# Optimization experiments

Measured on AMD Instinct MI355X. Metric: run time of the kernel, lower is better.

The kernel has to match this reference:

```python
import jax, jax.numpy as jnp
import numpy as np

K = 10  # num_neighbors in original nn_index call


def setup_inputs() -> dict:
    key = jax.random.key(0)
    k1, k2, k3, k4 = jax.random.split(key, 4)
    B, OBS, ACT, N = 256, 32, 2, 500000
    obs = jax.random.normal(k1, (B, OBS), dtype=jnp.float32)
    action = jax.random.normal(k2, (B, ACT), dtype=jnp.float32)
    mem_sa = jax.random.normal(k3, (N, OBS + ACT), dtype=jnp.float32)
    mem_Q = jax.random.normal(k4, (N, 1), dtype=jnp.float32)
    return {"obs": obs, "action": action, "mem_sa": mem_sa, "mem_Q": mem_Q}


def reference(obs, action, mem_sa, mem_Q):
    # query: [B, D] state-action, brute-force kNN over memory table [N, D]
    q = jnp.concatenate([obs, action], axis=1)
    # squared Euclidean distances (FLANN returns squared L2): [B, N]
    d2 = (jnp.sum(q * q, axis=1, keepdims=True)
          - 2.0 * q @ mem_sa.T
          + jnp.sum(mem_sa * mem_sa, axis=1)[None, :])
    neg_d, idx = jax.lax.top_k(-d2, K)   # nearest K neighbors
    dists = -neg_d                        # [B, K], ascending
    Qs = mem_Q[idx, 0]                    # gather Q values: [B, K]
    # NOTE: original applies softmax to raw distances (not negated)
    weights = jax.nn.softmax(dists, axis=1)
    return jnp.sum(weights * Qs, axis=1)  # [B]
```

## Files before the change

kernel.cpp:

```cpp
#include <hip/hip_runtime.h>
#include <hip/hip_bf16.h>
#include <math.h>

#define NPTS   500000
#define NB     256
#define TOPK   10
#define CAP    2048
#define SBLK   1024
#define SPER   16
#define MARGIN 2.0f
#define NWCH   15625
#define FBLK   1024
#define NSEG   4
#define LCAP   8
#define PMAIN  393216
#define OCAP   32768
#define CHB    4352

typedef short v2s  __attribute__((ext_vector_type(2)));
typedef short v4s  __attribute__((ext_vector_type(4)));
typedef short v8s  __attribute__((ext_vector_type(8)));
typedef float v16f __attribute__((ext_vector_type(16)));

__device__ __forceinline__ unsigned short f2bf(float f) {
    unsigned u = __float_as_uint(f);
    unsigned r = u + 0x7FFFu + ((u >> 16) & 1u);
    return (unsigned short)(r >> 16);
}
__device__ __forceinline__ float bf2f(unsigned short h) {
    return __uint_as_float(((unsigned)h) << 16);
}
__device__ __forceinline__ v2s pk2(float2 f) {
    __hip_bfloat162 h = __float22bfloat162_rn(f);
    v2s r;
    __builtin_memcpy(&r, &h, 4);
    return r;
}

__device__ __forceinline__ float norm34(const float* __restrict__ r) {
    float a0 = 0.f, a1 = 0.f, a2 = 0.f, a3 = 0.f;
#pragma unroll
    for (int d = 0; d < 32; d += 4) {
        a0 = fmaf(r[d + 0], r[d + 0], a0);
        a1 = fmaf(r[d + 1], r[d + 1], a1);
        a2 = fmaf(r[d + 2], r[d + 2], a2);
        a3 = fmaf(r[d + 3], r[d + 3], a3);
    }
    a0 = fmaf(r[32], r[32], a0);
    a1 = fmaf(r[33], r[33], a1);
    return (a0 + a1) + (a2 + a3);
}
__device__ __forceinline__ float dot34(const float* __restrict__ r, const float* q) {
    float a0 = 0.f, a1 = 0.f, a2 = 0.f, a3 = 0.f;
#pragma unroll
    for (int d = 0; d < 32; d += 4) {
        a0 = fmaf(r[d + 0], q[d + 0], a0);
        a1 = fmaf(r[d + 1], q[d + 1], a1);
        a2 = fmaf(r[d + 2], q[d + 2], a2);
        a3 = fmaf(r[d + 3], q[d + 3], a3);
    }
    a0 = fmaf(r[32], q[32], a0);
    a1 = fmaf(r[33], q[33], a1);
    return (a0 + a1) + (a2 + a3);
}
__device__ __forceinline__ float dot34_v4(const float4* __restrict__ r4, const float* q) {
    float a0 = 0.f, a1 = 0.f, a2 = 0.f, a3 = 0.f;
#pragma unroll
    for (int dp = 0; dp < 8; ++dp) {
        float4 v = r4[dp];
        a0 = fmaf(v.x, q[4 * dp + 0], a0);
        a1 = fmaf(v.y, q[4 * dp + 1], a1);
        a2 = fmaf(v.z, q[4 * dp + 2], a2);
        a3 = fmaf(v.w, q[4 * dp + 3], a3);
    }
    float2 t = *(const float2*)(r4 + 8);
    a0 = fmaf(t.x, q[32], a0);
    a1 = fmaf(t.y, q[33], a1);
    return (a0 + a1) + (a2 + a3);
}
__device__ __forceinline__ void load_q(const float* __restrict__ obs,
                                       const float* __restrict__ act, int b, float* q) {
#pragma unroll
    for (int d = 0; d < 32; ++d) q[d] = obs[b * 32 + d];
    q[32] = act[b * 2 + 0];
    q[33] = act[b * 2 + 1];
}

__global__ __launch_bounds__(256, 4) void k_sample(const float* __restrict__ obs,
                                                   const float* __restrict__ act,
                                                   const float* __restrict__ msa,
                                                   float* __restrict__ minima) {
    __shared__ __align__(16) float sm[SPER * 36];
    __shared__ float smn[SPER];
    const int g = blockIdx.x, t = threadIdx.x;
    const int base = g * SPER;
    for (int i = t; i < SPER * 34; i += 256) {
        int row = i / 34, d = i - row * 34;
        sm[row * 36 + d] = msa[(size_t)base * 34 + i];
    }
    __syncthreads();
    if (t < SPER) smn[t] = norm34(&sm[t * 36]);
    __syncthreads();
    float q[34];
    load_q(obs, act, t, q);
    float best = __builtin_inff();
#pragma unroll
    for (int j = 0; j < SPER; ++j) {
        float s = fmaf(-2.f, dot34_v4((const float4*)&sm[j * 36], q), smn[j]);
        best = fminf(best, s);
    }
    minima[(size_t)t * SBLK + g] = best;
}

__global__ __launch_bounds__(64) void k_tau(const float* __restrict__ minima,
                                            const float* __restrict__ obs,
                                            const float* __restrict__ act,
                                            v8s* __restrict__ afrag,
                                            int* __restrict__ cursor) {
    __shared__ __align__(16) unsigned short qs[48];
    const int b = blockIdx.x, lane = threadIdx.x;
    if (b == 0 && lane == 0) { cursor[0] = 0; cursor[1] = 0; }
    float v[16];
#pragma unroll
    for (int k = 0; k < 16; ++k) v[k] = minima[(size_t)b * SBLK + lane + 64 * k];
    float last = 0.f;
    for (int r = 0; r < TOPK; ++r) {
        float lm = v[0]; int la = 0;
#pragma unroll
        for (int k = 1; k < 16; ++k) { if (v[k] < lm) { lm = v[k]; la = k; } }
        float wm = lm;
        for (int off = 32; off; off >>= 1) wm = fminf(wm, __shfl_xor(wm, off));
        unsigned long long msk = __ballot(lm == wm);
        int first = (int)__builtin_ctzll(msk);
        if (lane == first) {
#pragma unroll
            for (int k = 0; k < 16; ++k) { if (k == la) v[k] = __builtin_inff(); }
        }
        last = wm;
    }
    float val = 0.f;
    if (lane < 32)       val = obs[b * 32 + lane];
    else if (lane < 34)  val = act[b * 2 + (lane - 32)];
    else if (lane == 34) val = -0.5f;
    else if (lane == 35) val = 0.5f * (last + MARGIN);
    if (lane < 48) qs[lane] = (lane < 36) ? f2bf(val) : (unsigned short)0;
    __syncthreads();
    if (lane < 6) {
        int s = lane >> 1, half = lane & 1;
        int qt = b >> 5, mrow = b & 31;
        v8s frag = *(const v8s*)&qs[s * 16 + half * 8];
        afrag[(qt * 3 + s) * 64 + half * 32 + mrow] = frag;
    }
}

__global__ __launch_bounds__(256, 4) void k_filter(const float* __restrict__ msa,
                                                   const v8s* __restrict__ afrag,
                                                   int* __restrict__ cursor,
                                                   unsigned* __restrict__ pbuf,
                                                   int* __restrict__ posq) {
    __shared__ __align__(16) float chunk[2][CHB / 4];
    __shared__ int lcount[NB];
    __shared__ int lcand[NB * LCAP];
    __shared__ int gbase;
    const int g = blockIdx.x, t = threadIdx.x;
    const int w = t >> 6, lane = t & 63;
    const int mrow = lane & 31, half = lane >> 5;
    v8s A[2][3];
#pragma unroll
    for (int j = 0; j < 2; ++j)
#pragma unroll
        for (int s = 0; s < 3; ++s)
            A[j][s] = afrag[((w * 2 + j) * 3 + s) * 64 + lane];
    lcount[t] = 0;
    const v16f zacc = (v16f)0.0f;

    float4 sreg; float treg = 0.f;
    const char* mb = (const char*)msa;
    auto stage_load = [&](int c) {
        const char* cb = mb + (size_t)c * CHB;
        sreg = *(const float4*)(cb + t * 16);
        if (t < 64) treg = *(const float*)(cb + 4096 + t * 4);
    };
    auto stage_write = [&](int nb) {
        *(float4*)((char*)&chunk[nb][0] + t * 16) = sreg;
        if (t < 64) *(float*)((char*)&chunk[nb][0] + 4096 + t * 4) = treg;
    };
    auto process = [&](int cur, int c) {
        const float* rp = &chunk[cur][0] + mrow * 34;
        const int p0 = c * 32 + mrow;
        float2 e0 = *(const float2*)(rp + half * 8 + 0);
        float2 e1 = *(const float2*)(rp + half * 8 + 2);
        float2 e2 = *(const float2*)(rp + half * 8 + 4);
        float2 e3 = *(const float2*)(rp + half * 8 + 6);
        float2 e4 = *(const float2*)(rp + 16 + half * 8 + 0);
        float2 e5 = *(const float2*)(rp + 16 + half * 8 + 2);
        float2 e6 = *(const float2*)(rp + 16 + half * 8 + 4);
        float2 e7 = *(const float2*)(rp + 16 + half * 8 + 6);
        float2 e8 = *(const float2*)(rp + 32);
        float n0 = 0.f, n1 = 0.f;
        n0 = fmaf(e0.x, e0.x, n0); n1 = fmaf(e0.y, e0.y, n1);
        n0 = fmaf(e1.x, e1.x, n0); n1 = fmaf(e1.y, e1.y, n1);
        n0 = fmaf(e2.x, e2.x, n0); n1 = fmaf(e2.y, e2.y, n1);
        n0 = fmaf(e3.x, e3.x, n0); n1 = fmaf(e3.y, e3.y, n1);
        n0 = fmaf(e4.x, e4.x, n0); n1 = fmaf(e4.y, e4.y, n1);
        n0 = fmaf(e5.x, e5.x, n0); n1 = fmaf(e5.y, e5.y, n1);
        n0 = fmaf(e6.x, e6.x, n0); n1 = fmaf(e6.y, e6.y, n1);
        n0 = fmaf(e7.x, e7.x, n0); n1 = fmaf(e7.y, e7.y, n1);
        float part = n0 + n1;
        part = fmaf(e8.x, e8.x * 0.5f, part);
        part = fmaf(e8.y, e8.y * 0.5f, part);
        float nrm = part + __shfl_xor(part, 32);
        float thr = 0.5f * nrm;
        v4s b0lo = __builtin_shufflevector(pk2(e0), pk2(e1), 0, 1, 2, 3);
        v4s b0hi = __builtin_shufflevector(pk2(e2), pk2(e3), 0, 1, 2, 3);
        v8s B0 = __builtin_shufflevector(b0lo, b0hi, 0, 1, 2, 3, 4, 5, 6, 7);
        v4s b1lo = __builtin_shufflevector(pk2(e4), pk2(e5), 0, 1, 2, 3);
        v4s b1hi = __builtin_shufflevector(pk2(e6), pk2(e7), 0, 1, 2, 3);
        v8s B1 = __builtin_shufflevector(b1lo, b1hi, 0, 1, 2, 3, 4, 5, 6, 7);
        v8s B2 = (v8s)(short)0;
        if (half == 0) {
            v2s m33 = pk2(e8);
            B2[0] = m33[0];
            B2[1] = m33[1];
            B2[3] = (short)0x3F80;
        }
#pragma unroll
        for (int j = 0; j < 2; ++j) {
            const int qt = w * 2 + j;
            v16f acc = __builtin_amdgcn_mfma_f32_32x32x16_bf16(A[j][0], B0, zacc, 0, 0, 0);
            acc = __builtin_amdgcn_mfma_f32_32x32x16_bf16(A[j][1], B1, acc, 0, 0, 0);
            acc = __builtin_amdgcn_mfma_f32_32x32x16_bf16(A[j][2], B2, acc, 0, 0, 0);
            float m0 = fmaxf(fmaxf(acc[0], acc[1]), acc[2]);
            float m1 = fmaxf(fmaxf(acc[3], acc[4]), acc[5]);
            float m2 = fmaxf(fmaxf(acc[6], acc[7]), acc[8]);
            float m3 = fmaxf(fmaxf(acc[9], acc[10]), acc[11]);
            float m4 = fmaxf(fmaxf(acc[12], acc[13]), acc[14]);
            float mx = fmaxf(fmaxf(fmaxf(m0, m1), m2),
                             fmaxf(fmaxf(m3, m4), acc[15]));
            if (mx >= thr) {
                unsigned hm = 0;
#pragma unroll
                for (int r = 0; r < 16; ++r) hm |= (acc[r] >= thr) ? (1u << r) : 0u;
                while (hm) {
                    int r = __builtin_ctz(hm);
                    hm &= hm - 1;
                    int qq = qt * 32 + (r & 3) + 8 * (r >> 2) + 4 * half;
                    int slot = atomicAdd(&lcount[qq], 1);
                    if (slot < LCAP) lcand[qq * LCAP + slot] = p0;
                    else {
                        int dg = atomicAdd(cursor + 1, 1);
                        if (dg < OCAP) pbuf[PMAIN + dg] = ((unsigned)qq << 19) | (unsigned)p0;
                    }
                }
            }
        }
    };

    int c = g;
    stage_load(c);
    stage_write(0);
    __syncthreads();
    int cur = 0;
#pragma unroll 1
    for (;;) {
        const int cn = c + FBLK;
        const bool hn = (cn < NWCH);
        if (hn) stage_load(cn);
        __builtin_amdgcn_sched_barrier(0);
        process(cur, c);
        if (!hn) break;
        stage_write(cur ^ 1);
        __syncthreads();
        cur ^= 1;
        c = cn;
    }
    __syncthreads();
    int n = lcount[t];
    if (n > LCAP) n = LCAP;
    lcount[t] = n;
    __syncthreads();
    for (int off = 1; off < 256; off <<= 1) {
        int v = (t >= off) ? lcount[t - off] : 0;
        __syncthreads();
        lcount[t] += v;
        __syncthreads();
    }
    int base_l = lcount[t] - n;
    if (t == 255) gbase = atomicAdd(cursor, lcount[255]);
    __syncthreads();
    int start = gbase + base_l;
    if (start >= PMAIN) { start = 0; n = 0; }
    else if (start + n > PMAIN) n = PMAIN - start;
    posq[g * NB + t] = start | (n << 20);
    for (int i = 0; i < n; ++i)
        pbuf[start + i] = (unsigned)lcand[t * LCAP + i];
}

__global__ __launch_bounds__(256) void k_final(const float* __restrict__ obs,
                                               const float* __restrict__ act,
                                               const float* __restrict__ msa,
                                               const unsigned* __restrict__ pbuf,
                                               const int* __restrict__ posq,
                                               const int* __restrict__ cursor,
                                               const float* __restrict__ memQ,
                                               float* __restrict__ out) {
    __shared__ float ls[CAP];
    __shared__ int   li[CAP];
    __shared__ int   sc[NB];
    __shared__ int   lcnt;
    __shared__ float rs[4];
    __shared__ int   ri[4];
    __shared__ float sel_s[TOPK];
    __shared__ int   sel_i[TOPK];
    const int b = blockIdx.x, t = threadIdx.x;
    const int lane = t & 63, wid = t >> 6;
    int nk[NSEG], pk6[NSEG], tot = 0;
#pragma unroll
    for (int k = 0; k < NSEG; ++k) {
        int packed = posq[(size_t)(t + 256 * k) * NB + b];
        nk[k] = (packed >> 20) & 0xF;
        pk6[k] = packed & 0xFFFFF;
        tot += nk[k];
    }
    sc[t] = tot;
    __syncthreads();
    for (int off = 1; off < 256; off <<= 1) {
        int v = (t >= off) ? sc[t - off] : 0;
        __syncthreads();
        sc[t] += v;
        __syncthreads();
    }
    int myoff = sc[t] - tot;
    if (t == 0) lcnt = (sc[255] > CAP) ? CAP : sc[255];
    __syncthreads();
#pragma unroll
    for (int k = 0; k < NSEG; ++k)
        for (int i = 0; i < nk[k]; ++i) {
            if (myoff < CAP) li[myoff] = (int)pbuf[pk6[k] + i];
            ++myoff;
        }
    int novf = cursor[1];
    if (novf > OCAP) novf = OCAP;
    for (int j = t; j < novf; j += 256) {
        unsigned pr = pbuf[PMAIN + j];
        if ((int)(pr >> 19) == b) {
            int s = atomicAdd(&lcnt, 1);
            if (s < CAP) li[s] = (int)(pr & 0x7FFFFu);
        }
    }
    __syncthreads();
    int cnt = lcnt;
    if (cnt > CAP) cnt = CAP;
    float q[34];
    load_q(obs, act, b, q);
    for (int j = t; j < cnt; j += 256) {
        const float* row = msa + (size_t)li[j] * 34;
        ls[j] = fmaf(-2.f, dot34(row, q), norm34(row));
    }
    __syncthreads();
    for (int k = 0; k < TOPK; ++k) {
        float bs = __builtin_inff();
        int   bi = 0x7fffffff;
        for (int j = t; j < cnt; j += 256) {
            float s = ls[j]; int i = li[j];
            if (s < bs || (s == bs && i < bi)) { bs = s; bi = i; }
        }
        for (int off = 32; off; off >>= 1) {
            float s2 = __shfl_down(bs, off);
            int   i2 = __shfl_down(bi, off);
            if (s2 < bs || (s2 == bs && i2 < bi)) { bs = s2; bi = i2; }
        }
        if (lane == 0) { rs[wid] = bs; ri[wid] = bi; }
        __syncthreads();
        if (t == 0) {
            float fs = rs[0]; int fi = ri[0];
#pragma unroll
            for (int ww = 1; ww < 4; ++ww) {
                if (rs[ww] < fs || (rs[ww] == fs && ri[ww] < fi)) { fs = rs[ww]; fi = ri[ww]; }
            }
            sel_s[k] = fs; sel_i[k] = fi;
        }
        __syncthreads();
        const int win = sel_i[k];
        for (int j = t; j < cnt; j += 256) {
            if (li[j] == win) ls[j] = __builtin_inff();
        }
        __syncthreads();
    }
    if (t == 0) {
        float m = sel_s[TOPK - 1];
        float wsum = 0.f, acc = 0.f;
#pragma unroll
        for (int k = 0; k < TOPK; ++k) {
            if (sel_i[k] == 0x7fffffff) continue;
            float w2 = expf(sel_s[k] - m);
            wsum += w2;
            acc = fmaf(w2, memQ[sel_i[k]], acc);
        }
        out[b] = acc / wsum;
    }
}

extern "C" void kernel_launch(void* const* d_in, const int* in_sizes, int n_in,
                              void* d_out, int out_size, void* d_ws, size_t ws_size,
                              hipStream_t stream) {
    const float* obs = (const float*)d_in[0];
    const float* act = (const float*)d_in[1];
    const float* msa = (const float*)d_in[2];
    const float* mq  = (const float*)d_in[3];
    float* out = (float*)d_out;

    char* ws = (char*)d_ws;
    int*      cursor = (int*)ws;
    v8s*      afrag  = (v8s*)(ws + 256);
    float*    minima = (float*)(ws + 32768);
    int*      posq   = (int*)(ws + 32768 + 1048576);
    unsigned* pbuf   = (unsigned*)(ws + 32768 + 1048576 + 1572864);

    k_sample<<<SBLK, 256, 0, stream>>>(obs, act, msa, minima);
    k_tau   <<<NB, 64, 0, stream>>>(minima, obs, act, afrag, cursor);
    k_filter<<<FBLK, 256, 0, stream>>>(msa, afrag, cursor, pbuf, posq);
    k_final <<<NB, 256, 0, stream>>>(obs, act, msa, pbuf, posq, cursor, mq, out);
}
```

Measured before the change: 171.6 us.

## Give each filter wave its own memory chunk across all query tiles

The filter kernel previously had all four waves share one 32-row chunk, each wave handling two of the eight query tiles. Now each wave processes its own chunk against all eight query tiles, with A fragments for every tile held in registers. Each block stages four chunks per round using wider float4 loads with bounds guards at the tail. The grid, segment count and occupancy bound are lowered to match. This cuts barriers and LDS staging per unit of work, at the cost of more registers and lower occupancy.

```diff
diff --git a/kernel.cpp b/kernel.cpp
--- a/kernel.cpp
+++ b/kernel.cpp
@@ -10,12 +10,14 @@
 #define SPER   16
 #define MARGIN 2.0f
 #define NWCH   15625
-#define FBLK   1024
-#define NSEG   4
+#define FBLK   768
+#define NSEG   3
 #define LCAP   8
 #define PMAIN  393216
 #define OCAP   32768
 #define CHB    4352
+#define RNDB   (4 * CHB)
+#define MSAB   68000000LL
 
 typedef short v2s  __attribute__((ext_vector_type(2)));
 typedef short v4s  __attribute__((ext_vector_type(4)));
@@ -153,40 +155,57 @@
     }
 }
 
-__global__ __launch_bounds__(256, 4) void k_filter(const float* __restrict__ msa,
+__global__ __launch_bounds__(256, 3) void k_filter(const float* __restrict__ msa,
                                                    const v8s* __restrict__ afrag,
                                                    int* __restrict__ cursor,
                                                    unsigned* __restrict__ pbuf,
                                                    int* __restrict__ posq) {
-    __shared__ __align__(16) float chunk[2][CHB / 4];
+    __shared__ __align__(16) float chunk[2][RNDB / 4];
     __shared__ int lcount[NB];
     __shared__ int lcand[NB * LCAP];
     __shared__ int gbase;
     const int g = blockIdx.x, t = threadIdx.x;
     const int w = t >> 6, lane = t & 63;
     const int mrow = lane & 31, half = lane >> 5;
-    v8s A[2][3];
-#pragma unroll
-    for (int j = 0; j < 2; ++j)
+    v8s A[8][3];
+#pragma unroll
+    for (int qt = 0; qt < 8; ++qt)
 #pragma unroll
         for (int s = 0; s < 3; ++s)
-            A[j][s] = afrag[((w * 2 + j) * 3 + s) * 64 + lane];
+            A[qt][s] = afrag[(qt * 3 + s) * 64 + lane];
     lcount[t] = 0;
     const v16f zacc = (v16f)0.0f;
-
-    float4 sreg; float treg = 0.f;
     const char* mb = (const char*)msa;
-    auto stage_load = [&](int c) {
-        const char* cb = mb + (size_t)c * CHB;
-        sreg = *(const float4*)(cb + t * 16);
-        if (t < 64) treg = *(const float*)(cb + 4096 + t * 4);
+
+    float4 s0, s1, s2, s3, s4;
+    auto stage_load = [&](int cb) {
+        const long long base = (long long)cb * CHB + (long long)t * 16;
+        if (cb + 4 <= NWCH) {
+            s0 = *(const float4*)(mb + base);
+            s1 = *(const float4*)(mb + base + 4096);
+            s2 = *(const float4*)(mb + base + 8192);
+            s3 = *(const float4*)(mb + base + 12288);
+            if (t < 64) s4 = *(const float4*)(mb + base + 16384);
+        } else {
+            s0 = s1 = s2 = s3 = s4 = (float4){0.f, 0.f, 0.f, 0.f};
+            if (base + 16 <= MSAB)          s0 = *(const float4*)(mb + base);
+            if (base + 4096 + 16 <= MSAB)   s1 = *(const float4*)(mb + base + 4096);
+            if (base + 8192 + 16 <= MSAB)   s2 = *(const float4*)(mb + base + 8192);
+            if (base + 12288 + 16 <= MSAB)  s3 = *(const float4*)(mb + base + 12288);
+            if (t < 64 && base + 16384 + 16 <= MSAB)
+                s4 = *(const float4*)(mb + base + 16384);
+        }
     };
     auto stage_write = [&](int nb) {
-        *(float4*)((char*)&chunk[nb][0] + t * 16) = sreg;
-        if (t < 64) *(float*)((char*)&chunk[nb][0] + 4096 + t * 4) = treg;
+        char* lb = (char*)&chunk[nb][0];
+        *(float4*)(lb + t * 16)         = s0;
+        *(float4*)(lb + t * 16 + 4096)  = s1;
+        *(float4*)(lb + t * 16 + 8192)  = s2;
+        *(float4*)(lb + t * 16 + 12288) = s3;
+        if (t < 64) *(float4*)(lb + t * 16 + 16384) = s4;
     };
     auto process = [&](int cur, int c) {
-        const float* rp = &chunk[cur][0] + mrow * 34;
+        const float* rp = &chunk[cur][0] + w * 1088 + mrow * 34;
         const int p0 = c * 32 + mrow;
         float2 e0 = *(const float2*)(rp + half * 8 + 0);
         float2 e1 = *(const float2*)(rp + half * 8 + 2);
@@ -225,11 +244,10 @@
             B2[3] = (short)0x3F80;
         }
 #pragma unroll
-        for (int j = 0; j < 2; ++j) {
-            const int qt = w * 2 + j;
-            v16f acc = __builtin_amdgcn_mfma_f32_32x32x16_bf16(A[j][0], B0, zacc, 0, 0, 0);
-            acc = __builtin_amdgcn_mfma_f32_32x32x16_bf16(A[j][1], B1, acc, 0, 0, 0);
-            acc = __builtin_amdgcn_mfma_f32_32x32x16_bf16(A[j][2], B2, acc, 0, 0, 0);
+        for (int qt = 0; qt < 8; ++qt) {
+            v16f acc = __builtin_amdgcn_mfma_f32_32x32x16_bf16(A[qt][0], B0, zacc, 0, 0, 0);
+            acc = __builtin_amdgcn_mfma_f32_32x32x16_bf16(A[qt][1], B1, acc, 0, 0, 0);
+            acc = __builtin_amdgcn_mfma_f32_32x32x16_bf16(A[qt][2], B2, acc, 0, 0, 0);
             float m0 = fmaxf(fmaxf(acc[0], acc[1]), acc[2]);
             float m1 = fmaxf(fmaxf(acc[3], acc[4]), acc[5]);
             float m2 = fmaxf(fmaxf(acc[6], acc[7]), acc[8]);
@@ -256,23 +274,24 @@
         }
     };
 
-    int c = g;
-    stage_load(c);
+    int cb = g * 4;
+    stage_load(cb);
     stage_write(0);
     __syncthreads();
     int cur = 0;
 #pragma unroll 1
     for (;;) {
-        const int cn = c + FBLK;
-        const bool hn = (cn < NWCH);
-        if (hn) stage_load(cn);
+        const int cbn = cb + FBLK * 4;
+        const bool hn = (cbn < NWCH);
+        if (hn) stage_load(cbn);
         __builtin_amdgcn_sched_barrier(0);
-        process(cur, c);
+        const int cw = cb + w;
+        if (cw < NWCH) process(cur, cw);
         if (!hn) break;
         stage_write(cur ^ 1);
         __syncthreads();
         cur ^= 1;
-        c = cn;
+        cb = cbn;
     }
     __syncthreads();
     int n = lcount[t];
```

New measurement: 172.1 us. No clear change (+0.3%).
